# Optimization experiments

Hardware: AMD Instinct MI355X
Metric: run time of the kernel (lower is better)

The kernel has to match this reference:

```python
import jax, jax.numpy as jnp
import numpy as np

B, D, K = 512, 128, 131072
TEMP = 0.07
PTR = 0  # queue_ptr starts at 0; B <= K so single contiguous write


def _normalize(x, axis):
    return x / jnp.linalg.norm(x, axis=axis, keepdims=True)


def setup_inputs() -> dict:
    key = jax.random.key(0)
    k = jax.random.split(key, 7)
    return {
        "predict0": jax.random.normal(k[0], (B, D), jnp.float32),
        "predict1": jax.random.normal(k[1], (B, D), jnp.float32),
        "project0": jax.random.normal(k[2], (B, D), jnp.float32),
        "project1": jax.random.normal(k[3], (B, D), jnp.float32),
        "queue": jax.random.normal(k[4], (D, K), jnp.float32),
        "queue_id": jax.random.randint(k[5], (K,), 0, 100000, jnp.int64) if jax.config.jax_enable_x64 else jax.random.randint(k[5], (K,), 0, 100000, jnp.int32),
        "ids": jax.random.randint(k[6], (B,), 0, 100000, jnp.int64) if jax.config.jax_enable_x64 else jax.random.randint(k[6], (B,), 0, 100000, jnp.int32),
    }


def _find_nn(proj, queue_n, queue_id, ids):
    # [B, K] similarity, mask out entries with same sample id, argmax, gather cols
    sim = proj @ queue_n                                   # [B, K]
    is_own = queue_id[None, :] == ids[:, None]             # [B, K]
    sim = jnp.where(is_own, jnp.float32(-1.0), sim)
    idx = jnp.argmax(sim, axis=1)                          # [B]
    return queue_n[:, idx]                                 # [D, B]


def _nnclr_loss(predicted, nn, temperature):
    # logits[i, j] = nn_i . predicted_j / T ; labels = arange(B)
    logits = (nn.T @ predicted.T) / temperature            # [B, B]
    logp = jax.nn.log_softmax(logits, axis=-1)
    return -jnp.mean(jnp.diagonal(logp))


def reference(predict0, predict1, project0, project1, queue, queue_id, ids):
    # forward_encoder's normalization (encoder itself is external and modeled out)
    p0 = _normalize(predict0, 1)
    p1 = _normalize(predict1, 1)
    z0 = _normalize(project0, 1)
    z1 = _normalize(project1, 1)
    queue_n = _normalize(queue, 0)  # queue stored normalized along dim 0

    # find_nn / queue are no_grad in the original
    nn0 = jax.lax.stop_gradient(_find_nn(jax.lax.stop_gradient(z0), queue_n, queue_id, ids))
    nn1 = jax.lax.stop_gradient(_find_nn(jax.lax.stop_gradient(z1), queue_n, queue_id, ids))

    loss0 = _nnclr_loss(p0, nn1, TEMP)
    loss1 = _nnclr_loss(p1, nn0, TEMP)
    loss = (loss0 + loss1) * 0.5

    # _dequeue_and_enqueue: ptr=0, B <= K -> contiguous slice write
    new_queue = jax.lax.dynamic_update_slice(queue_n, jax.lax.stop_gradient(z0.T), (0, PTR))
    new_queue_id = jax.lax.dynamic_update_slice(queue_id, ids, (PTR,))
    new_ptr = jnp.array((PTR + B) % K, dtype=queue_id.dtype)
    return loss, new_queue, new_queue_id, new_ptr
```

## Files before the change

kernel.cpp:

```cpp
#include <hip/hip_runtime.h>
#include <hip/hip_bf16.h>

typedef _Float16 half8 __attribute__((ext_vector_type(8)));
typedef _Float16 half4 __attribute__((ext_vector_type(4)));
typedef float f32x4 __attribute__((ext_vector_type(4)));

#define B 512
#define D 128
#define K 131072
#define TEMP 0.07f
#define NKB 512
#define KT_PER 16

#define INVN_OFF 0
#define Z0_OFF   131072
#define Z1_OFF   196608
#define P0_OFF   262144
#define P1_OFF   327680
#define ZF16_OFF 393216
#define QA_OFF   458752
#define PVAL_OFF 8847360
#define IDX_OFF  9371648
#define LP_OFF   9372672

__global__ __launch_bounds__(128) void rownorm_k(
    const float* __restrict__ p0, const float* __restrict__ p1,
    const float* __restrict__ z0, const float* __restrict__ z1,
    float* __restrict__ w, _Float16* __restrict__ zf16) {
  int row = blockIdx.x & (B - 1);
  int which = blockIdx.x >> 9;
  const float* src; float* dst;
  switch (which) {
    case 0: src = z0; dst = w + Z0_OFF; break;
    case 1: src = z1; dst = w + Z1_OFF; break;
    case 2: src = p0; dst = w + P0_OFF; break;
    default: src = p1; dst = w + P1_OFF; break;
  }
  int tid = threadIdx.x;
  float v = src[row * D + tid];
  float s = v * v;
  #pragma unroll
  for (int o = 32; o; o >>= 1) s += __shfl_xor(s, o);
  __shared__ float sm[2];
  if ((tid & 63) == 0) sm[tid >> 6] = s;
  __syncthreads();
  float inv = rsqrtf(sm[0] + sm[1]);
  float nv = v * inv;
  dst[row * D + tid] = nv;
  if (which < 2) zf16[(which * B + row) * D + tid] = (_Float16)nv;
}

__global__ __launch_bounds__(256) void colq_k(
    const float* __restrict__ q, const int* __restrict__ qid,
    const int* __restrict__ ids, const float* __restrict__ w_z0,
    float* __restrict__ invn, float* __restrict__ out,
    _Float16* __restrict__ qA) {
  __shared__ float psum[8][128];
  __shared__ float invs[128];
  __shared__ _Float16 tile[128][136];
  int tid = threadIdx.x;
  int kb = blockIdx.x;
  int k0 = kb * 128;
  {
    int kc = tid & 31, dg = tid >> 5;
    float4 acc = {0.f, 0.f, 0.f, 0.f};
    for (int i = 0; i < 16; i++) {
      int d = dg * 16 + i;
      float4 v = *(const float4*)(q + (size_t)d * K + k0 + kc * 4);
      acc.x = fmaf(v.x, v.x, acc.x); acc.y = fmaf(v.y, v.y, acc.y);
      acc.z = fmaf(v.z, v.z, acc.z); acc.w = fmaf(v.w, v.w, acc.w);
    }
    *(float4*)&psum[dg][kc * 4] = acc;
  }
  __syncthreads();
  if (tid < 128) {
    float s = 0.f;
    #pragma unroll
    for (int g2 = 0; g2 < 8; g2++) s += psum[g2][tid];
    float inv = rsqrtf(s);
    invs[tid] = inv;
    invn[k0 + tid] = inv;
    int kk = k0 + tid;
    out[1 + (size_t)D * K + kk] = (float)((kk < B) ? ids[kk] : qid[kk]);
  }
  __syncthreads();
  {
    int col = tid & 127, dh = tid >> 7;
    float inv = invs[col];
    const float* qc = q + k0 + col;
    float* oc = out + 1 + k0 + col;
    if (k0 < B) {
      const float* zc = w_z0 + (size_t)(k0 + col) * D;
      for (int i = 0; i < 64; i++) {
        int d = dh * 64 + i;
        float o = qc[(size_t)d * K] * inv;
        tile[d][col] = (_Float16)o;
        oc[(size_t)d * K] = zc[d];
      }
    } else {
      for (int i = 0; i < 64; i++) {
        int d = dh * 64 + i;
        float o = qc[(size_t)d * K] * inv;
        tile[d][col] = (_Float16)o;
        oc[(size_t)d * K] = o;
      }
    }
  }
  __syncthreads();
  {
    int dc = tid >> 6, l = tid & 63;
    int g = l >> 4, c = l & 15;
    #pragma unroll
    for (int kt = 0; kt < 8; kt++) {
      half8 f;
      #pragma unroll
      for (int i = 0; i < 8; i++) {
        int d = g * 4 + (i & 3) + ((i >> 2) << 4) + dc * 32;
        f[i] = tile[d][kt * 16 + c];
      }
      int ktg = kb * 8 + kt;
      *(half8*)(qA + (size_t)((ktg * 4 + dc) * 64 + l) * 8) = f;
    }
  }
}

#define LOADAF(AF, Q4, KTG) do { \
  _Pragma("unroll") \
  for (int dc = 0; dc < 4; dc++) \
    AF[dc] = *(const half8*)(qA + (size_t)(((KTG) * 4 + dc) * 64 + lane) * 8); \
  Q4 = *(const int4*)(qid + (KTG) * 16 + g * 4); \
} while (0)

#define PROCESS(AF, Q4, KTG) do { \
  int kbase = (KTG) * 16 + g * 4; \
  unsigned idxc0 = 0x1FFFFu - (unsigned)kbase; \
  _Pragma("unroll") \
  for (int nt = 0; nt < 4; nt++) { \
    f32x4 acc = {0.f, 0.f, 0.f, 0.f}; \
    _Pragma("unroll") \
    for (int dc = 0; dc < 4; dc++) \
      acc = __builtin_amdgcn_mfma_f32_16x16x32_f16(AF[dc], bf[nt][dc], acc, 0, 0, 0); \
    _Pragma("unroll") \
    for (int r = 0; r < 4; r++) { \
      float sv_ = acc[r]; \
      int qv_ = (r == 0) ? Q4.x : (r == 1) ? Q4.y : (r == 2) ? Q4.z : Q4.w; \
      float t_ = fmaf(sv_, 0.5f, 3.0f); \
      unsigned pk_ = ((__float_as_uint(t_) << 9) & 0xFFFE0000u) | (idxc0 - r); \
      pk_ = (qv_ == myid[nt]) ? 0u : pk_; \
      best[nt] = best[nt] > pk_ ? best[nt] : pk_; \
    } \
  } \
} while (0)

__global__ __launch_bounds__(256) void nnsearch_k(
    const _Float16* __restrict__ qA, const _Float16* __restrict__ zf16,
    const int* __restrict__ qid, const int* __restrict__ ids,
    unsigned* __restrict__ pbest) {
  int tid = threadIdx.x;
  int kb = blockIdx.x;
  int rg = blockIdx.y;
  int wave = tid >> 6, lane = tid & 63;
  int g = lane >> 4, c = lane & 15;
  int rowbase = rg * 256 + wave * 64;

  half8 bf[4][4];
  int myid[4];
  #pragma unroll
  for (int nt = 0; nt < 4; nt++) {
    int row = rowbase + nt * 16 + c;
    myid[nt] = ids[row & (B - 1)];
    #pragma unroll
    for (int dc = 0; dc < 4; dc++) {
      const _Float16* zr = zf16 + row * D + dc * 32 + g * 4;
      half4 lo = *(const half4*)zr;
      half4 hi = *(const half4*)(zr + 16);
      half8 f = {lo[0], lo[1], lo[2], lo[3], hi[0], hi[1], hi[2], hi[3]};
      bf[nt][dc] = f;
    }
  }

  unsigned best[4] = {0u, 0u, 0u, 0u};
  int kt0 = kb * KT_PER;
  half8 afA[4], afB[4];
  int4 q4A, q4B;
  LOADAF(afA, q4A, kt0);
  for (int kt = 0; kt < KT_PER; kt += 2) {
    LOADAF(afB, q4B, kt0 + kt + 1);
    PROCESS(afA, q4A, kt0 + kt);
    if (kt + 2 < KT_PER) LOADAF(afA, q4A, kt0 + kt + 2);
    PROCESS(afB, q4B, kt0 + kt + 1);
  }

  #pragma unroll
  for (int nt = 0; nt < 4; nt++) {
    unsigned v = best[nt];
    unsigned o1 = __shfl_xor(v, 16); v = v > o1 ? v : o1;
    unsigned o2 = __shfl_xor(v, 32); v = v > o2 ? v : o2;
    if (g == 0) {
      int row = rowbase + nt * 16 + c;
      pbest[row * NKB + kb] = v;
    }
  }
}

__global__ __launch_bounds__(256) void nnreduce_k(
    const unsigned* __restrict__ pbest, int* __restrict__ idxout) {
  int row = blockIdx.x;
  int tid = threadIdx.x;
  const unsigned* p = pbest + row * NKB;
  unsigned v = p[tid], u = p[tid + 256];
  v = v > u ? v : u;
  #pragma unroll
  for (int o = 32; o; o >>= 1) {
    unsigned ov = __shfl_xor(v, o);
    v = v > ov ? v : ov;
  }
  __shared__ unsigned sv[4];
  if ((tid & 63) == 0) sv[tid >> 6] = v;
  __syncthreads();
  if (tid == 0) {
    #pragma unroll
    for (int wv = 1; wv < 4; wv++) v = v > sv[wv] ? v : sv[wv];
    idxout[row] = (int)(0x1FFFFu - (v & 0x1FFFFu));
  }
}

__global__ __launch_bounds__(256) void loss_k(
    const float* __restrict__ q, const float* __restrict__ invn,
    const int* __restrict__ idxout, const float* __restrict__ w,
    float* __restrict__ lpart) {
  int i0 = blockIdx.x * 8;
  int v = blockIdx.y;
  int tid = threadIdx.x;
  __shared__ float nns[8][D];
  __shared__ float rm[8][4], re[8][4], sdlds[8];
  #pragma unroll
  for (int ii = 0; ii < 4; ii++) {
    int i = ii * 2 + (tid >> 7);
    int d = tid & 127;
    int nnidx = idxout[(v ? 0 : B) + i0 + i];
    nns[i][d] = q[(size_t)d * K + nnidx] * invn[nnidx];
  }
  __syncthreads();
  const float* pr = w + (v ? P1_OFF : P0_OFF);
  const float* r0 = pr + tid * D;
  const float* r1 = pr + (tid + 256) * D;
  float a0[8] = {0, 0, 0, 0, 0, 0, 0, 0};
  float a1[8] = {0, 0, 0, 0, 0, 0, 0, 0};
  for (int d = 0; d < D; d += 4) {
    float4 x0 = *(const float4*)(r0 + d);
    float4 x1 = *(const float4*)(r1 + d);
    #pragma unroll
    for (int i = 0; i < 8; i++) {
      float4 n = *(const float4*)&nns[i][d];
      a0[i] = fmaf(x0.x, n.x, a0[i]); a0[i] = fmaf(x0.y, n.y, a0[i]);
      a0[i] = fmaf(x0.z, n.z, a0[i]); a0[i] = fmaf(x0.w, n.w, a0[i]);
      a1[i] = fmaf(x1.x, n.x, a1[i]); a1[i] = fmaf(x1.y, n.y, a1[i]);
      a1[i] = fmaf(x1.z, n.z, a1[i]); a1[i] = fmaf(x1.w, n.w, a1[i]);
    }
  }
  #pragma unroll
  for (int i = 0; i < 8; i++) {
    a0[i] *= (1.0f / TEMP);
    a1[i] *= (1.0f / TEMP);
  }
  #pragma unroll
  for (int i = 0; i < 8; i++) {
    int ig = i0 + i;
    if ((ig & 256) == 0) { if (tid == ig) sdlds[i] = a0[i]; }
    else { if (tid == (ig & 255)) sdlds[i] = a1[i]; }
  }
  int wv = tid >> 6;
  #pragma unroll
  for (int i = 0; i < 8; i++) {
    float m = fmaxf(a0[i], a1[i]);
    #pragma unroll
    for (int o = 32; o; o >>= 1) m = fmaxf(m, __shfl_xor(m, o));
    if ((tid & 63) == 0) rm[i][wv] = m;
  }
  __syncthreads();
  #pragma unroll
  for (int i = 0; i < 8; i++) {
    float m = fmaxf(fmaxf(rm[i][0], rm[i][1]), fmaxf(rm[i][2], rm[i][3]));
    float e = expf(a0[i] - m) + expf(a1[i] - m);
    #pragma unroll
    for (int o = 32; o; o >>= 1) e += __shfl_xor(e, o);
    if ((tid & 63) == 0) re[i][wv] = e;
  }
  __syncthreads();
  if (tid < 8) {
    int i = tid;
    float m = fmaxf(fmaxf(rm[i][0], rm[i][1]), fmaxf(rm[i][2], rm[i][3]));
    float s = re[i][0] + re[i][1] + re[i][2] + re[i][3];
    lpart[v * B + i0 + i] = sdlds[i] - m - logf(s);
  }
}

__global__ __launch_bounds__(256) void final_k(
    const float* __restrict__ lpart, float* __restrict__ out) {
  int tid = threadIdx.x;
  float s = lpart[tid] + lpart[tid + 256] + lpart[tid + 512] + lpart[tid + 768];
  #pragma unroll
  for (int o = 32; o; o >>= 1) s += __shfl_xor(s, o);
  __shared__ float sm[4];
  if ((tid & 63) == 0) sm[tid >> 6] = s;
  __syncthreads();
  if (tid == 0) {
    float total = sm[0] + sm[1] + sm[2] + sm[3];
    out[0] = -total * (1.0f / 1024.0f);
    out[1 + D * K + K] = 512.0f;
  }
}

extern "C" void kernel_launch(void* const* d_in, const int* in_sizes, int n_in,
                              void* d_out, int out_size, void* d_ws, size_t ws_size,
                              hipStream_t stream) {
  const float* p0 = (const float*)d_in[0];
  const float* p1 = (const float*)d_in[1];
  const float* z0 = (const float*)d_in[2];
  const float* z1 = (const float*)d_in[3];
  const float* q  = (const float*)d_in[4];
  const int* qid  = (const int*)d_in[5];
  const int* ids  = (const int*)d_in[6];
  float* out = (float*)d_out;
  float* w = (float*)d_ws;
  float* invn = w + INVN_OFF;
  _Float16* zf16 = (_Float16*)(w + ZF16_OFF);
  _Float16* qA   = (_Float16*)(w + QA_OFF);
  unsigned* pbest = (unsigned*)(w + PVAL_OFF);
  int* idxout = (int*)(w + IDX_OFF);
  float* lpart = w + LP_OFF;

  rownorm_k<<<2048, 128, 0, stream>>>(p0, p1, z0, z1, w, zf16);
  colq_k<<<K / 128, 256, 0, stream>>>(q, qid, ids, w + Z0_OFF, invn, out, qA);
  dim3 g(NKB, 4);
  nnsearch_k<<<g, 256, 0, stream>>>(qA, zf16, qid, ids, pbest);
  nnreduce_k<<<1024, 256, 0, stream>>>(pbest, idxout);
  dim3 gl(B / 8, 2);
  loss_k<<<gl, 256, 0, stream>>>(q, invn, idxout, w, lpart);
  final_k<<<1, 256, 0, stream>>>(lpart, out);
}
```

Measured before the change: 131.7 us.

## Track float max in NN search and recover argmax index in a fix-up pass

The inner loop of the nearest-neighbour search now keeps only a float running max (a select plus fmaxf) instead of packing the score and index into an unsigned key each step. The reduce kernel finds the winning k-block from the per-block maxima. A new nnfix_k kernel then recomputes that block's 16 tiles and picks the smallest index whose score equals the max. This removes per-element integer packing ALU work from the hot MFMA loop, at the cost of an extra kernel launch and a small recompute. It also changes tie-breaking and the quantisation of the comparison from a truncated key to an exact float compare.

Measured after the change: 135.2 us. 2.7% more time.

```diff
diff --git a/kernel.cpp b/kernel.cpp
--- a/kernel.cpp
+++ b/kernel.cpp
@@ -20,8 +20,10 @@
 #define ZF16_OFF 393216
 #define QA_OFF   458752
 #define PVAL_OFF 8847360
-#define IDX_OFF  9371648
-#define LP_OFF   9372672
+#define WKB_OFF  9371648
+#define WVAL_OFF 9372672
+#define IDX_OFF  9373696
+#define LP_OFF   9374720
 
 __global__ __launch_bounds__(128) void rownorm_k(
     const float* __restrict__ p0, const float* __restrict__ p1,
@@ -132,8 +134,6 @@
 } while (0)
 
 #define PROCESS(AF, Q4, KTG) do { \
-  int kbase = (KTG) * 16 + g * 4; \
-  unsigned idxc0 = 0x1FFFFu - (unsigned)kbase; \
   _Pragma("unroll") \
   for (int nt = 0; nt < 4; nt++) { \
     f32x4 acc = {0.f, 0.f, 0.f, 0.f}; \
@@ -142,12 +142,9 @@
       acc = __builtin_amdgcn_mfma_f32_16x16x32_f16(AF[dc], bf[nt][dc], acc, 0, 0, 0); \
     _Pragma("unroll") \
     for (int r = 0; r < 4; r++) { \
-      float sv_ = acc[r]; \
       int qv_ = (r == 0) ? Q4.x : (r == 1) ? Q4.y : (r == 2) ? Q4.z : Q4.w; \
-      float t_ = fmaf(sv_, 0.5f, 3.0f); \
-      unsigned pk_ = ((__float_as_uint(t_) << 9) & 0xFFFE0000u) | (idxc0 - r); \
-      pk_ = (qv_ == myid[nt]) ? 0u : pk_; \
-      best[nt] = best[nt] > pk_ ? best[nt] : pk_; \
+      float sm_ = (qv_ == myid[nt]) ? -1.0f : acc[r]; \
+      best[nt] = fmaxf(best[nt], sm_); \
     } \
   } \
 } while (0)
@@ -155,7 +152,7 @@
 __global__ __launch_bounds__(256) void nnsearch_k(
     const _Float16* __restrict__ qA, const _Float16* __restrict__ zf16,
     const int* __restrict__ qid, const int* __restrict__ ids,
-    unsigned* __restrict__ pbest) {
+    float* __restrict__ pval) {
   int tid = threadIdx.x;
   int kb = blockIdx.x;
   int rg = blockIdx.y;
@@ -179,7 +176,7 @@
     }
   }
 
-  unsigned best[4] = {0u, 0u, 0u, 0u};
+  float best[4] = {-2.f, -2.f, -2.f, -2.f};
   int kt0 = kb * KT_PER;
   half8 afA[4], afB[4];
   int4 q4A, q4B;
@@ -193,23 +190,26 @@
 
   #pragma unroll
   for (int nt = 0; nt < 4; nt++) {
-    unsigned v = best[nt];
-    unsigned o1 = __shfl_xor(v, 16); v = v > o1 ? v : o1;
-    unsigned o2 = __shfl_xor(v, 32); v = v > o2 ? v : o2;
+    float v = best[nt];
+    v = fmaxf(v, __shfl_xor(v, 16));
+    v = fmaxf(v, __shfl_xor(v, 32));
     if (g == 0) {
       int row = rowbase + nt * 16 + c;
-      pbest[row * NKB + kb] = v;
+      pval[row * NKB + kb] = v;
     }
   }
 }
 
 __global__ __launch_bounds__(256) void nnreduce_k(
-    const unsigned* __restrict__ pbest, int* __restrict__ idxout) {
+    const float* __restrict__ pval, int* __restrict__ wkb,
+    float* __restrict__ wval) {
   int row = blockIdx.x;
   int tid = threadIdx.x;
-  const unsigned* p = pbest + row * NKB;
-  unsigned v = p[tid], u = p[tid + 256];
-  v = v > u ? v : u;
+  const float* p = pval + row * NKB;
+  float a = p[tid], b = p[tid + 256];
+  unsigned pa = (__float_as_uint(fmaf(a, 0.5f, 3.0f)) << 9) | (unsigned)(511 - tid);
+  unsigned pb = (__float_as_uint(fmaf(b, 0.5f, 3.0f)) << 9) | (unsigned)(255 - tid);
+  unsigned v = pa > pb ? pa : pb;
   #pragma unroll
   for (int o = 32; o; o >>= 1) {
     unsigned ov = __shfl_xor(v, o);
@@ -221,8 +221,61 @@
   if (tid == 0) {
     #pragma unroll
     for (int wv = 1; wv < 4; wv++) v = v > sv[wv] ? v : sv[wv];
-    idxout[row] = (int)(0x1FFFFu - (v & 0x1FFFFu));
-  }
+    int kb = 511 - (int)(v & 0x1FFu);
+    wkb[row] = kb;
+    wval[row] = pval[row * NKB + kb];
+  }
+}
+
+__global__ __launch_bounds__(256) void nnfix_k(
+    const _Float16* __restrict__ qA, const _Float16* __restrict__ zf16,
+    const int* __restrict__ qid, const int* __restrict__ ids,
+    const int* __restrict__ wkb, const float* __restrict__ wval,
+    int* __restrict__ idxout) {
+  int tid = threadIdx.x;
+  int wave = tid >> 6, lane = tid & 63;
+  int g = lane >> 4;
+  int row = blockIdx.x * 4 + wave;
+  int kb = wkb[row];
+  float wv = wval[row];
+  int myid = ids[row & (B - 1)];
+
+  half8 bf[4];
+  #pragma unroll
+  for (int dc = 0; dc < 4; dc++) {
+    const _Float16* zr = zf16 + row * D + dc * 32 + g * 4;
+    half4 lo = *(const half4*)zr;
+    half4 hi = *(const half4*)(zr + 16);
+    half8 f = {lo[0], lo[1], lo[2], lo[3], hi[0], hi[1], hi[2], hi[3]};
+    bf[dc] = f;
+  }
+
+  unsigned kbest = 0x7FFFFFFFu;
+  int kt0 = kb * KT_PER;
+  for (int kt = 0; kt < KT_PER; kt++) {
+    int ktg = kt0 + kt;
+    half8 af[4];
+    #pragma unroll
+    for (int dc = 0; dc < 4; dc++)
+      af[dc] = *(const half8*)(qA + (size_t)((ktg * 4 + dc) * 64 + lane) * 8);
+    int4 q4 = *(const int4*)(qid + ktg * 16 + g * 4);
+    f32x4 acc = {0.f, 0.f, 0.f, 0.f};
+    #pragma unroll
+    for (int dc = 0; dc < 4; dc++)
+      acc = __builtin_amdgcn_mfma_f32_16x16x32_f16(af[dc], bf[dc], acc, 0, 0, 0);
+    #pragma unroll
+    for (int r = 0; r < 4; r++) {
+      int qv = (r == 0) ? q4.x : (r == 1) ? q4.y : (r == 2) ? q4.z : q4.w;
+      float sm = (qv == myid) ? -1.0f : acc[r];
+      if (sm == wv) {
+        unsigned kk = (unsigned)(ktg * 16 + g * 4 + r);
+        kbest = kbest < kk ? kbest : kk;
+      }
+    }
+  }
+  unsigned o1 = __shfl_xor(kbest, 16); kbest = kbest < o1 ? kbest : o1;
+  unsigned o2 = __shfl_xor(kbest, 32); kbest = kbest < o2 ? kbest : o2;
+  if (lane == 0) idxout[row] = (int)(kbest < (K - 1) ? kbest : (K - 1));
 }
 
 __global__ __launch_bounds__(256) void loss_k(
@@ -327,15 +380,18 @@
   float* invn = w + INVN_OFF;
   _Float16* zf16 = (_Float16*)(w + ZF16_OFF);
   _Float16* qA   = (_Float16*)(w + QA_OFF);
-  unsigned* pbest = (unsigned*)(w + PVAL_OFF);
+  float* pval = w + PVAL_OFF;
+  int* wkb    = (int*)(w + WKB_OFF);
+  float* wval = w + WVAL_OFF;
   int* idxout = (int*)(w + IDX_OFF);
   float* lpart = w + LP_OFF;
 
   rownorm_k<<<2048, 128, 0, stream>>>(p0, p1, z0, z1, w, zf16);
   colq_k<<<K / 128, 256, 0, stream>>>(q, qid, ids, w + Z0_OFF, invn, out, qA);
   dim3 g(NKB, 4);
-  nnsearch_k<<<g, 256, 0, stream>>>(qA, zf16, qid, ids, pbest);
-  nnreduce_k<<<1024, 256, 0, stream>>>(pbest, idxout);
+  nnsearch_k<<<g, 256, 0, stream>>>(qA, zf16, qid, ids, pval);
+  nnreduce_k<<<1024, 256, 0, stream>>>(pval, wkb, wval);
+  nnfix_k<<<256, 256, 0, stream>>>(qA, zf16, qid, ids, wkb, wval, idxout);
   dim3 gl(B / 8, 2);
   loss_k<<<gl, 256, 0, stream>>>(q, invn, idxout, w, lpart);
   final_k<<<1, 256, 0, stream>>>(lpart, out);
```
